# Kernel tuning notes

Hardware: AMD Instinct MI355X
Metric: run time of the kernel (lower is better)

## Reference

```python
import jax, jax.numpy as jnp
import numpy as np

H_MODEL = 1024
N_HEADS = 16
N_KV_HEADS = 4
HEAD_DIM = 64
SLIDING_WINDOW = 512
B, S = 2, 2048
NEG_INF = -1e9


def rotate_half(x):
    half = x.shape[-1] // 2
    return jnp.concatenate([-x[..., half:], x[..., :half]], axis=-1)


def setup_inputs() -> dict:
    key = jax.random.key(0)
    ks = jax.random.split(key, 8)
    hidden_states = jax.random.normal(ks[0], (B, S, H_MODEL), dtype=jnp.float32)
    # RoPE tables (HF style): cos/sin of shape [1, S, head_dim]
    inv_freq = 1.0 / (10000.0 ** (jnp.arange(0, HEAD_DIM, 2, dtype=jnp.float32) / HEAD_DIM))
    pos = jnp.arange(S, dtype=jnp.float32)
    freqs = jnp.einsum('s,d->sd', pos, inv_freq)            # [S, D/2]
    emb = jnp.concatenate([freqs, freqs], axis=-1)          # [S, D]
    cos = jnp.cos(emb)[None]                                # [1, S, D]
    sin = jnp.sin(emb)[None]
    # additive causal + sliding-window mask [1,1,S,S]
    i = jnp.arange(S)[:, None]
    j = jnp.arange(S)[None, :]
    allowed = (j <= i) & (i - j < SLIDING_WINDOW)
    attention_mask = jnp.where(allowed, 0.0, NEG_INF).astype(jnp.float32)[None, None]
    # projection weights (torch Linear stores [out, in]; y = x @ W.T)
    std = 0.02
    Wq = jax.random.normal(ks[1], (N_HEADS * HEAD_DIM, H_MODEL), dtype=jnp.float32) * std
    Wk = jax.random.normal(ks[2], (N_KV_HEADS * HEAD_DIM, H_MODEL), dtype=jnp.float32) * std
    Wv = jax.random.normal(ks[3], (N_KV_HEADS * HEAD_DIM, H_MODEL), dtype=jnp.float32) * std
    Wo = jax.random.normal(ks[4], (H_MODEL, N_HEADS * HEAD_DIM), dtype=jnp.float32) * std
    return {"hidden_states": hidden_states, "cos": cos, "sin": sin,
            "attention_mask": attention_mask, "Wq": Wq, "Wk": Wk, "Wv": Wv, "Wo": Wo}


def reference(hidden_states, cos, sin, attention_mask, Wq, Wk, Wv, Wo):
    b, s, _ = hidden_states.shape
    G = N_HEADS // N_KV_HEADS
    scaling = HEAD_DIM ** -0.5
    # QKV projections -> [B, H, S, D]
    q = jnp.einsum('bsh,oh->bso', hidden_states, Wq).reshape(b, s, N_HEADS, HEAD_DIM).transpose(0, 2, 1, 3)
    k = jnp.einsum('bsh,oh->bso', hidden_states, Wk).reshape(b, s, N_KV_HEADS, HEAD_DIM).transpose(0, 2, 1, 3)
    v = jnp.einsum('bsh,oh->bso', hidden_states, Wv).reshape(b, s, N_KV_HEADS, HEAD_DIM).transpose(0, 2, 1, 3)
    # RoPE (cos/sin broadcast over head dim via unsqueeze(1))
    c = cos[:, None, :, :]
    sn = sin[:, None, :, :]
    q = q * c + rotate_half(q) * sn
    k = k * c + rotate_half(k) * sn
    # GQA eager attention: group query heads over kv heads
    qg = q.reshape(b, N_KV_HEADS, G, s, HEAD_DIM)
    scores = jnp.einsum('bkgqd,bkpd->bkgqp', qg, k) * scaling  # [B,Hkv,G,S,S]
    scores = scores + attention_mask[:, :, None, :, :]
    probs = jax.nn.softmax(scores.astype(jnp.float32), axis=-1).astype(q.dtype)
    out = jnp.einsum('bkgqp,bkpd->bkgqd', probs, v)            # [B,Hkv,G,S,D]
    out = out.reshape(b, N_HEADS, s, HEAD_DIM).transpose(0, 2, 1, 3).reshape(b, s, N_HEADS * HEAD_DIM)
    return jnp.einsum('bso,ho->bsh', out, Wo)
```

## Files before the change

kernel.cpp:

```cpp
#include <hip/hip_runtime.h>
#include <hip/hip_bf16.h>

#define S_LEN 2048
#define NH 16
#define NKV 4
#define HD 64
#define WIN 512
#define BATCH 2

typedef __bf16 bf16_8 __attribute__((ext_vector_type(8)));
typedef __bf16 bf16_4 __attribute__((ext_vector_type(4)));
typedef float f32x4 __attribute__((ext_vector_type(4)));

__device__ inline bf16_8 cvt8(f32x4 a, f32x4 b) {
    bf16_8 r;
    r[0] = (__bf16)a[0]; r[1] = (__bf16)a[1]; r[2] = (__bf16)a[2]; r[3] = (__bf16)a[3];
    r[4] = (__bf16)b[0]; r[5] = (__bf16)b[1]; r[6] = (__bf16)b[2]; r[7] = (__bf16)b[3];
    return r;
}

__global__ __launch_bounds__(256) void cvt_pack(
    const float* __restrict__ hs, const float* __restrict__ Wq,
    const float* __restrict__ Wk, const float* __restrict__ Wv,
    const float* __restrict__ Wo,
    __bf16* __restrict__ hsb, __bf16* __restrict__ Wqp,
    __bf16* __restrict__ Wkp, __bf16* __restrict__ Wvp,
    __bf16* __restrict__ Wop)
{
    int i = blockIdx.x * 256 + threadIdx.x;
    if (i < 524288) {
        const size_t j = (size_t)i * 8;
        const f32x4 a = *(const f32x4*)(hs + j);
        const f32x4 b = *(const f32x4*)(hs + j + 4);
        *(bf16_8*)(hsb + j) = cvt8(a, b);
        return;
    }
    i -= 524288;
    const float* S; __bf16* P;
    if (i < 131072)      { S = Wq; P = Wqp; }
    else if (i < 163840) { S = Wk; P = Wkp; i -= 131072; }
    else if (i < 196608) { S = Wv; P = Wvp; i -= 163840; }
    else                 { S = Wo; P = Wop; i -= 196608; }
    const int n = i >> 7;
    const int k = (i & 127) << 3;
    const f32x4 a = *(const f32x4*)(S + (size_t)n * 1024 + k);
    const f32x4 b = *(const f32x4*)(S + (size_t)n * 1024 + k + 4);
    const size_t dst = ((size_t)((n >> 4) * 32 + (k >> 5)) << 9)
                     + ((size_t)((n & 15) | (((k >> 3) & 3) << 4)) << 3);
    *(bf16_8*)(P + dst) = cvt8(a, b);
}

#define GEMM_K_LOOP(Ap_, Bq_, row0_)                                           \
    const int ar = tid >> 2, ac = (tid & 3) << 4;                              \
    const int fm = lane & 15;                                                  \
    const int fj = (lane >> 4) << 3;                                           \
    const f32x4 fzero = {0.f, 0.f, 0.f, 0.f};                                  \
    f32x4 acc[2][4];                                                           \
    _Pragma("unroll") for (int i = 0; i < 2; ++i)                              \
        _Pragma("unroll") for (int nt = 0; nt < 4; ++nt) acc[i][nt] = fzero;   \
    const size_t aoff = (size_t)(row0_ + ar) * 1024 + ac;                      \
    bf16_8 b0[4], b1[4];                                                       \
    {                                                                          \
        const bf16_8 a0 = *(const bf16_8*)&Ap_[aoff];                          \
        const bf16_8 a1 = *(const bf16_8*)&Ap_[aoff + 8];                      \
        *(bf16_8*)&As[ar * 72 + ac]     = a0;                                  \
        *(bf16_8*)&As[ar * 72 + ac + 8] = a1;                                  \
        _Pragma("unroll") for (int nt = 0; nt < 4; ++nt)                       \
            b0[nt] = *(const bf16_8*)(Bq_ + nt * 16384);                       \
    }                                                                          \
    __syncthreads();                                                           \
    for (int it = 0; it < 16; ++it) {                                          \
        const int cur = it & 1;                                                \
        const bool pf = it < 15;                                               \
        bf16_8 qa0, qa1, bn[4];                                                \
        if (pf) {                                                              \
            qa0 = *(const bf16_8*)&Ap_[aoff + (it + 1) * 64];                  \
            qa1 = *(const bf16_8*)&Ap_[aoff + (it + 1) * 64 + 8];              \
        }                                                                      \
        _Pragma("unroll") for (int nt = 0; nt < 4; ++nt)                       \
            b1[nt] = *(const bf16_8*)(Bq_ + nt * 16384 + (it * 2 + 1) * 512);  \
        bf16_8 af0[2];                                                         \
        _Pragma("unroll") for (int i = 0; i < 2; ++i)                          \
            af0[i] = *(const bf16_8*)&As[cur * 4608 + (wm * 32 + i * 16 + fm) * 72 + fj]; \
        _Pragma("unroll") for (int i = 0; i < 2; ++i)                          \
            _Pragma("unroll") for (int nt = 0; nt < 4; ++nt)                   \
                acc[i][nt] = __builtin_amdgcn_mfma_f32_16x16x32_bf16(          \
                    af0[i], b0[nt], acc[i][nt], 0, 0, 0);                      \
        if (pf) {                                                              \
            _Pragma("unroll") for (int nt = 0; nt < 4; ++nt)                   \
                bn[nt] = *(const bf16_8*)(Bq_ + nt * 16384 + (it + 1) * 1024); \
        }                                                                      \
        bf16_8 af1[2];                                                         \
        _Pragma("unroll") for (int i = 0; i < 2; ++i)                          \
            af1[i] = *(const bf16_8*)&As[cur * 4608 + (wm * 32 + i * 16 + fm) * 72 + 32 + fj]; \
        _Pragma("unroll") for (int i = 0; i < 2; ++i)                          \
            _Pragma("unroll") for (int nt = 0; nt < 4; ++nt)                   \
                acc[i][nt] = __builtin_amdgcn_mfma_f32_16x16x32_bf16(          \
                    af1[i], b1[nt], acc[i][nt], 0, 0, 0);                      \
        if (pf) {                                                              \
            const int nb = cur ^ 1;                                            \
            *(bf16_8*)&As[nb * 4608 + ar * 72 + ac]     = qa0;                 \
            *(bf16_8*)&As[nb * 4608 + ar * 72 + ac + 8] = qa1;                 \
            _Pragma("unroll") for (int nt = 0; nt < 4; ++nt) b0[nt] = bn[nt];  \
        }                                                                      \
        __syncthreads();                                                       \
    }                                                                          \
    const int drow = (lane >> 4) << 2;

__global__ __launch_bounds__(256) void gemm_qkv(
    const __bf16* __restrict__ A,
    const __bf16* __restrict__ Wqp,
    const __bf16* __restrict__ Wkp,
    const __bf16* __restrict__ Wvp,
    __bf16* __restrict__ Qb,
    __bf16* __restrict__ Kb,
    __bf16* __restrict__ Vt,
    const float* __restrict__ cosb,
    const float* __restrict__ sinb)
{
    __shared__ __align__(16) __bf16 smem[9216];
    __bf16* const As = smem;

    const int tid  = threadIdx.x;
    const int wave = tid >> 6;
    const int lane = tid & 63;
    const int wm   = wave & 1;
    const int wn   = wave >> 1;

    const int row0 = blockIdx.x * 64;
    const int by   = blockIdx.y;

    const __bf16* Bp; int colb; int mode;
    __bf16* C; int ldc; int col0;
    if (by < 8)       { Bp = Wqp; colb = by * 128;        C = Qb; ldc = 1024; col0 = by * 128;        mode = 0; }
    else if (by < 10) { Bp = Wkp; colb = (by - 8) * 128;  C = Kb; ldc = 256;  col0 = (by - 8) * 128;  mode = 1; }
    else              { Bp = Wvp; colb = (by - 10) * 128; C = 0;  ldc = 0;    col0 = (by - 10) * 128; mode = 2; }

    const __bf16* Bq = Bp + (size_t)((colb + wn * 64) >> 4) * 16384 + (lane << 3);

    GEMM_K_LOOP(A, Bq, row0)

    const int cq = col0 + wn * 64;
    if (mode < 2) {
#pragma unroll
        for (int i = 0; i < 2; ++i) {
#pragma unroll
            for (int r = 0; r < 4; ++r) {
                const int row = row0 + wm * 32 + i * 16 + drow + r;
                const int s   = row & (S_LEN - 1);
#pragma unroll
                for (int nt = 0; nt < 2; ++nt) {
                    const int d = nt * 16 + fm;
                    const float c1 = cosb[s * HD + d];
                    const float s1 = sinb[s * HD + d];
                    const float c2 = cosb[s * HD + d + 32];
                    const float s2 = sinb[s * HD + d + 32];
                    const float x1 = acc[i][nt][r];
                    const float x2 = acc[i][nt + 2][r];
                    C[(size_t)row * ldc + cq + d]      = (__bf16)(x1 * c1 - x2 * s1);
                    C[(size_t)row * ldc + cq + d + 32] = (__bf16)(x2 * c2 + x1 * s2);
                }
            }
        }
    } else {
        __bf16* T = smem;
#pragma unroll
        for (int i = 0; i < 2; ++i)
#pragma unroll
            for (int r = 0; r < 4; ++r)
#pragma unroll
                for (int nt = 0; nt < 4; ++nt)
                    T[(wn * 64 + nt * 16 + fm) * 72 + wm * 32 + i * 16 + drow + r] =
                        (__bf16)acc[i][nt][r];
        __syncthreads();
        const int nl = tid >> 1;
        const int so = (tid & 1) << 5;
        const int ng = col0 + nl;
        const int kh = ng >> 6, d = ng & 63;
        const int b  = row0 >> 11, s0v = row0 & (S_LEN - 1);
        __bf16* dst = &Vt[(size_t)((b * NKV + kh) * HD + d) * S_LEN + s0v + so];
#pragma unroll
        for (int c = 0; c < 4; ++c)
            *(bf16_8*)(dst + c * 8) = *(const bf16_8*)&T[nl * 72 + so + c * 8];
    }
}

__global__ __launch_bounds__(256) void gemm_o(
    const __bf16* __restrict__ A,
    const __bf16* __restrict__ Bp,
    float* __restrict__ C)
{
    __shared__ __align__(16) __bf16 smem[9216];
    __bf16* const As = smem;

    const int tid  = threadIdx.x;
    const int wave = tid >> 6;
    const int lane = tid & 63;
    const int wm   = wave & 1;
    const int wn   = wave >> 1;

    const int row0 = blockIdx.x * 64;
    const int colb = blockIdx.y * 128;

    const __bf16* Bq = Bp + (size_t)((colb + wn * 64) >> 4) * 16384 + (lane << 3);

    GEMM_K_LOOP(A, Bq, row0)

#pragma unroll
    for (int i = 0; i < 2; ++i)
#pragma unroll
        for (int r = 0; r < 4; ++r) {
            const int row = row0 + wm * 32 + i * 16 + drow + r;
#pragma unroll
            for (int nt = 0; nt < 4; ++nt)
                C[(size_t)row * 1024 + colb + wn * 64 + nt * 16 + fm] = acc[i][nt][r];
        }
}

__global__ __launch_bounds__(256) void attn_mfma(const __bf16* __restrict__ Q,
                                                 const __bf16* __restrict__ K,
                                                 const __bf16* __restrict__ Vt,
                                                 __bf16* __restrict__ O)
{
    __shared__ __align__(16) __bf16 Ks[64 * 72];
    __shared__ __align__(16) __bf16 Vs[64 * 72];
    __shared__ __align__(16) __bf16 Ps[4][16][72];

    const int tid  = threadIdx.x;
    const int wave = tid >> 6;
    const int lane = tid & 63;

    const int qt = blockIdx.x & (S_LEN / 64 - 1);
    const int h  = (blockIdx.x >> 5) & (NH - 1);
    const int b  = blockIdx.x >> 9;
    const int kh = h >> 2;

    const int q0 = qt * 64;
    const int qw = q0 + wave * 16;

    const int fm = lane & 15;
    const int fj = (lane >> 4) << 3;

    const size_t qrow = (size_t)(b * S_LEN + qw + fm) * (NH * HD) + h * HD;
    const bf16_8 qf0 = *(const bf16_8*)&Q[qrow + fj];
    const bf16_8 qf1 = *(const bf16_8*)&Q[qrow + 32 + fj];

    const f32x4 fzero = {0.f, 0.f, 0.f, 0.f};
    f32x4 oacc[4];
    float l[4];
#pragma unroll
    for (int nt = 0; nt < 4; ++nt) oacc[nt] = fzero;
#pragma unroll
    for (int r = 0; r < 4; ++r) l[r] = 0.f;

    const int kr = tid >> 3;
    const int kc = (tid & 7) << 3;
    const size_t kbase = (size_t)(b * S_LEN + kr) * (NKV * HD) + kh * HD + kc;
    const size_t vbase = (size_t)((b * NKV + kh) * HD + kr) * S_LEN + kc;
    const int qbase = qw + ((lane >> 4) << 2);

    const int lo  = (q0 >= WIN) ? (q0 - WIN) : 0;
    const int nit = ((q0 - lo) >> 6) + 1;

    bf16_8 pk0 = *(const bf16_8*)&K[kbase + (size_t)lo * (NKV * HD)];
    bf16_8 pk1 = *(const bf16_8*)&K[kbase + (size_t)(lo + 32) * (NKV * HD)];
    bf16_8 pv0 = *(const bf16_8*)&Vt[vbase + lo];
    bf16_8 pv1 = *(const bf16_8*)&Vt[vbase + (size_t)32 * S_LEN + lo];

    for (int it = 0; it < nit; ++it) {
        const int kb = lo + (it << 6);
        *(bf16_8*)&Ks[kr * 72 + kc]        = pk0;
        *(bf16_8*)&Ks[(kr + 32) * 72 + kc] = pk1;
        *(bf16_8*)&Vs[kr * 72 + kc]        = pv0;
        *(bf16_8*)&Vs[(kr + 32) * 72 + kc] = pv1;
        __syncthreads();

        if (it + 1 < nit) {
            const int kn = kb + 64;
            pk0 = *(const bf16_8*)&K[kbase + (size_t)kn * (NKV * HD)];
            pk1 = *(const bf16_8*)&K[kbase + (size_t)(kn + 32) * (NKV * HD)];
            pv0 = *(const bf16_8*)&Vt[vbase + kn];
            pv1 = *(const bf16_8*)&Vt[vbase + (size_t)32 * S_LEN + kn];
        }

        if (kb <= qw + 15 && (qw - kb) < (WIN + 63)) {
            f32x4 sc[4];
#pragma unroll
            for (int t = 0; t < 4; ++t) {
                const bf16_8 klo = *(const bf16_8*)&Ks[(t * 16 + fm) * 72 + fj];
                const bf16_8 khi = *(const bf16_8*)&Ks[(t * 16 + fm) * 72 + 32 + fj];
                f32x4 s = fzero;
                s = __builtin_amdgcn_mfma_f32_16x16x32_bf16(qf0, klo, s, 0, 0, 0);
                s = __builtin_amdgcn_mfma_f32_16x16x32_bf16(qf1, khi, s, 0, 0, 0);
                sc[t] = s;
            }

#pragma unroll
            for (int t = 0; t < 4; ++t) {
                const int ki = kb + t * 16 + fm;
#pragma unroll
                for (int r = 0; r < 4; ++r) {
                    const int qr = qbase + r;
                    const float e = __expf(sc[t][r] * 0.125f);
                    const float p = (ki <= qr && qr - ki < WIN) ? e : 0.f;
                    l[r] += p;
                    Ps[wave][((lane >> 4) << 2) + r][t * 16 + fm] = (__bf16)p;
                }
            }

            const bf16_8 pf0 = *(const bf16_8*)&Ps[wave][fm][fj];
            const bf16_8 pf1 = *(const bf16_8*)&Ps[wave][fm][32 + fj];
#pragma unroll
            for (int nt = 0; nt < 4; ++nt) {
                const bf16_8 vlo = *(const bf16_8*)&Vs[(nt * 16 + fm) * 72 + fj];
                const bf16_8 vhi = *(const bf16_8*)&Vs[(nt * 16 + fm) * 72 + 32 + fj];
                oacc[nt] = __builtin_amdgcn_mfma_f32_16x16x32_bf16(pf0, vlo, oacc[nt], 0, 0, 0);
                oacc[nt] = __builtin_amdgcn_mfma_f32_16x16x32_bf16(pf1, vhi, oacc[nt], 0, 0, 0);
            }
        }
        __syncthreads();
    }

#pragma unroll
    for (int off = 8; off > 0; off >>= 1)
#pragma unroll
        for (int r = 0; r < 4; ++r)
            l[r] += __shfl_xor(l[r], off, 64);

    const int drow = (lane >> 4) << 2;
    float inv[4];
#pragma unroll
    for (int r = 0; r < 4; ++r) inv[r] = 1.0f / l[r];
#pragma unroll
    for (int nt = 0; nt < 4; ++nt)
#pragma unroll
        for (int r = 0; r < 4; ++r) {
            const size_t off = (size_t)(b * S_LEN + qw + drow + r) * (NH * HD) + h * HD + nt * 16 + fm;
            O[off] = (__bf16)(oacc[nt][r] * inv[r]);
        }
}

extern "C" void kernel_launch(void* const* d_in, const int* in_sizes, int n_in,
                              void* d_out, int out_size, void* d_ws, size_t ws_size,
                              hipStream_t stream)
{
    const float* hs   = (const float*)d_in[0];
    const float* cosb = (const float*)d_in[1];
    const float* sinb = (const float*)d_in[2];
    const float* Wq = (const float*)d_in[4];
    const float* Wk = (const float*)d_in[5];
    const float* Wv = (const float*)d_in[6];
    const float* Wo = (const float*)d_in[7];

    const int M = BATCH * S_LEN;

    __bf16* hsb = (__bf16*)d_ws;
    __bf16* Wqp = hsb + (size_t)M * 1024;
    __bf16* Wkp = Wqp + 1024 * 1024;
    __bf16* Wvp = Wkp + 256 * 1024;
    __bf16* Wop = Wvp + 256 * 1024;
    __bf16* Qb  = Wop + 1024 * 1024;
    __bf16* Kb  = Qb  + (size_t)M * 1024;
    __bf16* Vtb = Kb  + (size_t)M * 256;
    __bf16* Ob  = Vtb + (size_t)M * 256;

    dim3 blk(256);
    cvt_pack<<<3328, blk, 0, stream>>>(hs, Wq, Wk, Wv, Wo,
                                       hsb, Wqp, Wkp, Wvp, Wop);

    gemm_qkv<<<dim3(64, 12), blk, 0, stream>>>(hsb, Wqp, Wkp, Wvp,
                                               Qb, Kb, Vtb, cosb, sinb);

    attn_mfma<<<BATCH * NH * (S_LEN / 64), blk, 0, stream>>>(Qb, Kb, Vtb, Ob);

    gemm_o<<<dim3(64, 8), blk, 0, stream>>>(Ob, Wop, (float*)d_out);
}
```

Baseline: 160.6 us.

## Fuse all four kernels into one persistent cooperative kernel with grid syncs

Replaces the four launches (convert/pack, QKV GEMM with RoPE, attention, output GEMM) with a single cooperative kernel of 512 persistent blocks. The stages are separated by grid.sync() and each block loops over tiles. The aim is to remove per-launch overhead and the idle gaps between kernels. In exchange, the grid is fixed at 512 blocks, so the attention stage runs 4 tiles serially per block and load balance changes. Grid-wide barriers cost something, and occupancy is constrained by launch_bounds(256,2) and a larger shared-memory footprint.

```diff
diff --git a/kernel.cpp b/kernel.cpp
--- a/kernel.cpp
+++ b/kernel.cpp
@@ -1,5 +1,8 @@
 #include <hip/hip_runtime.h>
 #include <hip/hip_bf16.h>
+#include <hip/hip_cooperative_groups.h>
+
+namespace cg = cooperative_groups;
 
 #define S_LEN 2048
 #define NH 16
@@ -7,9 +10,9 @@
 #define HD 64
 #define WIN 512
 #define BATCH 2
+#define GRID 512
 
 typedef __bf16 bf16_8 __attribute__((ext_vector_type(8)));
-typedef __bf16 bf16_4 __attribute__((ext_vector_type(4)));
 typedef float f32x4 __attribute__((ext_vector_type(4)));
 
 __device__ inline bf16_8 cvt8(f32x4 a, f32x4 b) {
@@ -19,325 +22,325 @@
     return r;
 }
 
-__global__ __launch_bounds__(256) void cvt_pack(
-    const float* __restrict__ hs, const float* __restrict__ Wq,
-    const float* __restrict__ Wk, const float* __restrict__ Wv,
-    const float* __restrict__ Wo,
+__device__ __forceinline__ void gemm64x128(
+    const __bf16* __restrict__ Ap, const __bf16* __restrict__ Bq,
+    int row0, __bf16* __restrict__ As, int tid, f32x4 acc[2][4])
+{
+    const int wave = tid >> 6;
+    const int lane = tid & 63;
+    const int wm   = wave & 1;
+    const int ar = tid >> 2, ac = (tid & 3) << 4;
+    const int fm = lane & 15;
+    const int fj = (lane >> 4) << 3;
+    const f32x4 fzero = {0.f, 0.f, 0.f, 0.f};
+#pragma unroll
+    for (int i = 0; i < 2; ++i)
+#pragma unroll
+        for (int nt = 0; nt < 4; ++nt) acc[i][nt] = fzero;
+
+    const size_t aoff = (size_t)(row0 + ar) * 1024 + ac;
+    bf16_8 b0[4], b1[4];
+    {
+        const bf16_8 a0 = *(const bf16_8*)&Ap[aoff];
+        const bf16_8 a1 = *(const bf16_8*)&Ap[aoff + 8];
+        *(bf16_8*)&As[ar * 72 + ac]     = a0;
+        *(bf16_8*)&As[ar * 72 + ac + 8] = a1;
+#pragma unroll
+        for (int nt = 0; nt < 4; ++nt)
+            b0[nt] = *(const bf16_8*)(Bq + nt * 16384);
+    }
+    __syncthreads();
+
+    for (int it = 0; it < 16; ++it) {
+        const int cur = it & 1;
+        const bool pf = it < 15;
+        bf16_8 qa0, qa1, bn[4];
+        if (pf) {
+            qa0 = *(const bf16_8*)&Ap[aoff + (it + 1) * 64];
+            qa1 = *(const bf16_8*)&Ap[aoff + (it + 1) * 64 + 8];
+        }
+#pragma unroll
+        for (int nt = 0; nt < 4; ++nt)
+            b1[nt] = *(const bf16_8*)(Bq + nt * 16384 + (it * 2 + 1) * 512);
+
+        bf16_8 af0[2];
+#pragma unroll
+        for (int i = 0; i < 2; ++i)
+            af0[i] = *(const bf16_8*)&As[cur * 4608 + (wm * 32 + i * 16 + fm) * 72 + fj];
+#pragma unroll
+        for (int i = 0; i < 2; ++i)
+#pragma unroll
+            for (int nt = 0; nt < 4; ++nt)
+                acc[i][nt] = __builtin_amdgcn_mfma_f32_16x16x32_bf16(af0[i], b0[nt], acc[i][nt], 0, 0, 0);
+
+        if (pf) {
+#pragma unroll
+            for (int nt = 0; nt < 4; ++nt)
+                bn[nt] = *(const bf16_8*)(Bq + nt * 16384 + (it + 1) * 1024);
+        }
+        bf16_8 af1[2];
+#pragma unroll
+        for (int i = 0; i < 2; ++i)
+            af1[i] = *(const bf16_8*)&As[cur * 4608 + (wm * 32 + i * 16 + fm) * 72 + 32 + fj];
+#pragma unroll
+        for (int i = 0; i < 2; ++i)
+#pragma unroll
+            for (int nt = 0; nt < 4; ++nt)
+                acc[i][nt] = __builtin_amdgcn_mfma_f32_16x16x32_bf16(af1[i], b1[nt], acc[i][nt], 0, 0, 0);
+
+        if (pf) {
+            const int nb = cur ^ 1;
+            *(bf16_8*)&As[nb * 4608 + ar * 72 + ac]     = qa0;
+            *(bf16_8*)&As[nb * 4608 + ar * 72 + ac + 8] = qa1;
+#pragma unroll
+            for (int nt = 0; nt < 4; ++nt) b0[nt] = bn[nt];
+        }
+        __syncthreads();
+    }
+}
+
+__global__ __launch_bounds__(256, 2) void fused_all(
+    const float* __restrict__ hs,  const float* __restrict__ cosb,
+    const float* __restrict__ sinb,
+    const float* __restrict__ Wq,  const float* __restrict__ Wk,
+    const float* __restrict__ Wv,  const float* __restrict__ Wo,
     __bf16* __restrict__ hsb, __bf16* __restrict__ Wqp,
     __bf16* __restrict__ Wkp, __bf16* __restrict__ Wvp,
-    __bf16* __restrict__ Wop)
+    __bf16* __restrict__ Wop,
+    __bf16* __restrict__ Qb,  __bf16* __restrict__ Kb,
+    __bf16* __restrict__ Vt,  __bf16* __restrict__ Ob,
+    float* __restrict__ outp)
 {
-    int i = blockIdx.x * 256 + threadIdx.x;
-    if (i < 524288) {
-        const size_t j = (size_t)i * 8;
-        const f32x4 a = *(const f32x4*)(hs + j);
-        const f32x4 b = *(const f32x4*)(hs + j + 4);
-        *(bf16_8*)(hsb + j) = cvt8(a, b);
-        return;
-    }
-    i -= 524288;
-    const float* S; __bf16* P;
-    if (i < 131072)      { S = Wq; P = Wqp; }
-    else if (i < 163840) { S = Wk; P = Wkp; i -= 131072; }
-    else if (i < 196608) { S = Wv; P = Wvp; i -= 163840; }
-    else                 { S = Wo; P = Wop; i -= 196608; }
-    const int n = i >> 7;
-    const int k = (i & 127) << 3;
-    const f32x4 a = *(const f32x4*)(S + (size_t)n * 1024 + k);
-    const f32x4 b = *(const f32x4*)(S + (size_t)n * 1024 + k + 4);
-    const size_t dst = ((size_t)((n >> 4) * 32 + (k >> 5)) << 9)
-                     + ((size_t)((n & 15) | (((k >> 3) & 3) << 4)) << 3);
-    *(bf16_8*)(P + dst) = cvt8(a, b);
-}
-
-#define GEMM_K_LOOP(Ap_, Bq_, row0_)                                           \
-    const int ar = tid >> 2, ac = (tid & 3) << 4;                              \
-    const int fm = lane & 15;                                                  \
-    const int fj = (lane >> 4) << 3;                                           \
-    const f32x4 fzero = {0.f, 0.f, 0.f, 0.f};                                  \
-    f32x4 acc[2][4];                                                           \
-    _Pragma("unroll") for (int i = 0; i < 2; ++i)                              \
-        _Pragma("unroll") for (int nt = 0; nt < 4; ++nt) acc[i][nt] = fzero;   \
-    const size_t aoff = (size_t)(row0_ + ar) * 1024 + ac;                      \
-    bf16_8 b0[4], b1[4];                                                       \
-    {                                                                          \
-        const bf16_8 a0 = *(const bf16_8*)&Ap_[aoff];                          \
-        const bf16_8 a1 = *(const bf16_8*)&Ap_[aoff + 8];                      \
-        *(bf16_8*)&As[ar * 72 + ac]     = a0;                                  \
-        *(bf16_8*)&As[ar * 72 + ac + 8] = a1;                                  \
-        _Pragma("unroll") for (int nt = 0; nt < 4; ++nt)                       \
-            b0[nt] = *(const bf16_8*)(Bq_ + nt * 16384);                       \
-    }                                                                          \
-    __syncthreads();                                                           \
-    for (int it = 0; it < 16; ++it) {                                          \
-        const int cur = it & 1;                                                \
-        const bool pf = it < 15;                                               \
-        bf16_8 qa0, qa1, bn[4];                                                \
-        if (pf) {                                                              \
-            qa0 = *(const bf16_8*)&Ap_[aoff + (it + 1) * 64];                  \
-            qa1 = *(const bf16_8*)&Ap_[aoff + (it + 1) * 64 + 8];              \
-        }                                                                      \
-        _Pragma("unroll") for (int nt = 0; nt < 4; ++nt)                       \
-            b1[nt] = *(const bf16_8*)(Bq_ + nt * 16384 + (it * 2 + 1) * 512);  \
-        bf16_8 af0[2];                                                         \
-        _Pragma("unroll") for (int i = 0; i < 2; ++i)                          \
-            af0[i] = *(const bf16_8*)&As[cur * 4608 + (wm * 32 + i * 16 + fm) * 72 + fj]; \
-        _Pragma("unroll") for (int i = 0; i < 2; ++i)                          \
-            _Pragma("unroll") for (int nt = 0; nt < 4; ++nt)                   \
-                acc[i][nt] = __builtin_amdgcn_mfma_f32_16x16x32_bf16(          \
-                    af0[i], b0[nt], acc[i][nt], 0, 0, 0);                      \
-        if (pf) {                                                              \
-            _Pragma("unroll") for (int nt = 0; nt < 4; ++nt)                   \
-                bn[nt] = *(const bf16_8*)(Bq_ + nt * 16384 + (it + 1) * 1024); \
-        }                                                                      \
-        bf16_8 af1[2];                                                         \
-        _Pragma("unroll") for (int i = 0; i < 2; ++i)                          \
-            af1[i] = *(const bf16_8*)&As[cur * 4608 + (wm * 32 + i * 16 + fm) * 72 + 32 + fj]; \
-        _Pragma("unroll") for (int i = 0; i < 2; ++i)                          \
-            _Pragma("unroll") for (int nt = 0; nt < 4; ++nt)                   \
-                acc[i][nt] = __builtin_amdgcn_mfma_f32_16x16x32_bf16(          \
-                    af1[i], b1[nt], acc[i][nt], 0, 0, 0);                      \
-        if (pf) {                                                              \
-            const int nb = cur ^ 1;                                            \
-            *(bf16_8*)&As[nb * 4608 + ar * 72 + ac]     = qa0;                 \
-            *(bf16_8*)&As[nb * 4608 + ar * 72 + ac + 8] = qa1;                 \
-            _Pragma("unroll") for (int nt = 0; nt < 4; ++nt) b0[nt] = bn[nt];  \
-        }                                                                      \
-        __syncthreads();                                                       \
-    }                                                                          \
-    const int drow = (lane >> 4) << 2;
-
-__global__ __launch_bounds__(256) void gemm_qkv(
-    const __bf16* __restrict__ A,
-    const __bf16* __restrict__ Wqp,
-    const __bf16* __restrict__ Wkp,
-    const __bf16* __restrict__ Wvp,
-    __bf16* __restrict__ Qb,
-    __bf16* __restrict__ Kb,
-    __bf16* __restrict__ Vt,
-    const float* __restrict__ cosb,
-    const float* __restrict__ sinb)
-{
-    __shared__ __align__(16) __bf16 smem[9216];
-    __bf16* const As = smem;
+    __shared__ __align__(16) __bf16 smem[13824];
+    cg::grid_group grid = cg::this_grid();
 
     const int tid  = threadIdx.x;
+    const int bid  = blockIdx.x;
     const int wave = tid >> 6;
     const int lane = tid & 63;
     const int wm   = wave & 1;
     const int wn   = wave >> 1;
-
-    const int row0 = blockIdx.x * 64;
-    const int by   = blockIdx.y;
-
-    const __bf16* Bp; int colb; int mode;
-    __bf16* C; int ldc; int col0;
-    if (by < 8)       { Bp = Wqp; colb = by * 128;        C = Qb; ldc = 1024; col0 = by * 128;        mode = 0; }
-    else if (by < 10) { Bp = Wkp; colb = (by - 8) * 128;  C = Kb; ldc = 256;  col0 = (by - 8) * 128;  mode = 1; }
-    else              { Bp = Wvp; colb = (by - 10) * 128; C = 0;  ldc = 0;    col0 = (by - 10) * 128; mode = 2; }
-
-    const __bf16* Bq = Bp + (size_t)((colb + wn * 64) >> 4) * 16384 + (lane << 3);
-
-    GEMM_K_LOOP(A, Bq, row0)
-
-    const int cq = col0 + wn * 64;
-    if (mode < 2) {
-#pragma unroll
-        for (int i = 0; i < 2; ++i) {
+    const int fm   = lane & 15;
+    const int fj   = (lane >> 4) << 3;
+
+    for (int i0 = bid * 256 + tid; i0 < 851968; i0 += GRID * 256) {
+        int i = i0;
+        if (i < 524288) {
+            const size_t j = (size_t)i * 8;
+            const f32x4 a = *(const f32x4*)(hs + j);
+            const f32x4 b = *(const f32x4*)(hs + j + 4);
+            *(bf16_8*)(hsb + j) = cvt8(a, b);
+            continue;
+        }
+        i -= 524288;
+        const float* S; __bf16* P;
+        if (i < 131072)      { S = Wq; P = Wqp; }
+        else if (i < 163840) { S = Wk; P = Wkp; i -= 131072; }
+        else if (i < 196608) { S = Wv; P = Wvp; i -= 163840; }
+        else                 { S = Wo; P = Wop; i -= 196608; }
+        const int n = i >> 7;
+        const int k = (i & 127) << 3;
+        const f32x4 a = *(const f32x4*)(S + (size_t)n * 1024 + k);
+        const f32x4 b = *(const f32x4*)(S + (size_t)n * 1024 + k + 4);
+        const size_t dst = ((size_t)((n >> 4) * 32 + (k >> 5)) << 9)
+                         + ((size_t)((n & 15) | (((k >> 3) & 3) << 4)) << 3);
+        *(bf16_8*)(P + dst) = cvt8(a, b);
+    }
+    grid.sync();
+
+    for (int t = bid; t < 768; t += GRID) {
+        const int row0 = (t & 63) * 64;
+        const int by   = t >> 6;
+
+        const __bf16* Bp; int colb; int mode;
+        __bf16* C; int ldc; int col0;
+        if (by < 8)       { Bp = Wqp; colb = by * 128;        C = Qb; ldc = 1024; col0 = by * 128;        mode = 0; }
+        else if (by < 10) { Bp = Wkp; colb = (by - 8) * 128;  C = Kb; ldc = 256;  col0 = (by - 8) * 128;  mode = 1; }
+        else              { Bp = Wvp; colb = (by - 10) * 128; C = 0;  ldc = 0;    col0 = (by - 10) * 128; mode = 2; }
+
+        const __bf16* Bq = Bp + (size_t)((colb + wn * 64) >> 4) * 16384 + (lane << 3);
+        f32x4 acc[2][4];
+        gemm64x128(hsb, Bq, row0, smem, tid, acc);
+
+        const int drow = (lane >> 4) << 2;
+        const int cq   = col0 + wn * 64;
+        if (mode < 2) {
+#pragma unroll
+            for (int i = 0; i < 2; ++i) {
+#pragma unroll
+                for (int r = 0; r < 4; ++r) {
+                    const int row = row0 + wm * 32 + i * 16 + drow + r;
+                    const int s   = row & (S_LEN - 1);
+#pragma unroll
+                    for (int nt = 0; nt < 2; ++nt) {
+                        const int d = nt * 16 + fm;
+                        const float c1 = cosb[s * HD + d];
+                        const float s1 = sinb[s * HD + d];
+                        const float c2 = cosb[s * HD + d + 32];
+                        const float s2 = sinb[s * HD + d + 32];
+                        const float x1 = acc[i][nt][r];
+                        const float x2 = acc[i][nt + 2][r];
+                        C[(size_t)row * ldc + cq + d]      = (__bf16)(x1 * c1 - x2 * s1);
+                        C[(size_t)row * ldc + cq + d + 32] = (__bf16)(x2 * c2 + x1 * s2);
+                    }
+                }
+            }
+        } else {
+            __bf16* T = smem;
+#pragma unroll
+            for (int i = 0; i < 2; ++i)
+#pragma unroll
+                for (int r = 0; r < 4; ++r)
+#pragma unroll
+                    for (int nt = 0; nt < 4; ++nt)
+                        T[(wn * 64 + nt * 16 + fm) * 72 + wm * 32 + i * 16 + drow + r] =
+                            (__bf16)acc[i][nt][r];
+            __syncthreads();
+            const int nl = tid >> 1;
+            const int so = (tid & 1) << 5;
+            const int ng = col0 + nl;
+            const int kh = ng >> 6, d = ng & 63;
+            const int b  = row0 >> 11, s0v = row0 & (S_LEN - 1);
+            __bf16* dst = &Vt[(size_t)((b * NKV + kh) * HD + d) * S_LEN + s0v + so];
+#pragma unroll
+            for (int c = 0; c < 4; ++c)
+                *(bf16_8*)(dst + c * 8) = *(const bf16_8*)&T[nl * 72 + so + c * 8];
+        }
+        __syncthreads();
+    }
+    grid.sync();
+
+    {
+        __bf16* const Ks = smem;
+        __bf16* const Vs = smem + 4608;
+        __bf16* const Ps = smem + 9216;
+
+        for (int t = bid * 4; t < bid * 4 + 4; ++t) {
+            const int qt = t & (S_LEN / 64 - 1);
+            const int h  = (t >> 5) & (NH - 1);
+            const int b  = t >> 9;
+            const int kh = h >> 2;
+
+            const int q0 = qt * 64;
+            const int qw = q0 + wave * 16;
+
+            const size_t qrow = (size_t)(b * S_LEN + qw + fm) * (NH * HD) + h * HD;
+            const bf16_8 qf0 = *(const bf16_8*)&Qb[qrow + fj];
+            const bf16_8 qf1 = *(const bf16_8*)&Qb[qrow + 32 + fj];
+
+            const f32x4 fzero = {0.f, 0.f, 0.f, 0.f};
+            f32x4 oacc[4];
+            float l[4];
+#pragma unroll
+            for (int nt = 0; nt < 4; ++nt) oacc[nt] = fzero;
+#pragma unroll
+            for (int r = 0; r < 4; ++r) l[r] = 0.f;
+
+            const int kr = tid >> 3;
+            const int kc = (tid & 7) << 3;
+            const size_t kbase = (size_t)(b * S_LEN + kr) * (NKV * HD) + kh * HD + kc;
+            const size_t vbase = (size_t)((b * NKV + kh) * HD + kr) * S_LEN + kc;
+            const int qbase = qw + ((lane >> 4) << 2);
+
+            const int lo  = (q0 >= WIN) ? (q0 - WIN) : 0;
+            const int nit = ((q0 - lo) >> 6) + 1;
+
+            bf16_8 pk0 = *(const bf16_8*)&Kb[kbase + (size_t)lo * (NKV * HD)];
+            bf16_8 pk1 = *(const bf16_8*)&Kb[kbase + (size_t)(lo + 32) * (NKV * HD)];
+            bf16_8 pv0 = *(const bf16_8*)&Vt[vbase + lo];
+            bf16_8 pv1 = *(const bf16_8*)&Vt[vbase + (size_t)32 * S_LEN + lo];
+
+            for (int it = 0; it < nit; ++it) {
+                const int kb = lo + (it << 6);
+                *(bf16_8*)&Ks[kr * 72 + kc]        = pk0;
+                *(bf16_8*)&Ks[(kr + 32) * 72 + kc] = pk1;
+                *(bf16_8*)&Vs[kr * 72 + kc]        = pv0;
+                *(bf16_8*)&Vs[(kr + 32) * 72 + kc] = pv1;
+                __syncthreads();
+
+                if (it + 1 < nit) {
+                    const int kn = kb + 64;
+                    pk0 = *(const bf16_8*)&Kb[kbase + (size_t)kn * (NKV * HD)];
+                    pk1 = *(const bf16_8*)&Kb[kbase + (size_t)(kn + 32) * (NKV * HD)];
+                    pv0 = *(const bf16_8*)&Vt[vbase + kn];
+                    pv1 = *(const bf16_8*)&Vt[vbase + (size_t)32 * S_LEN + kn];
+                }
+
+                if (kb <= qw + 15 && (qw - kb) < (WIN + 63)) {
+                    f32x4 sc[4];
+#pragma unroll
+                    for (int tt = 0; tt < 4; ++tt) {
+                        const bf16_8 klo = *(const bf16_8*)&Ks[(tt * 16 + fm) * 72 + fj];
+                        const bf16_8 khi = *(const bf16_8*)&Ks[(tt * 16 + fm) * 72 + 32 + fj];
+                        f32x4 s = fzero;
+                        s = __builtin_amdgcn_mfma_f32_16x16x32_bf16(qf0, klo, s, 0, 0, 0);
+                        s = __builtin_amdgcn_mfma_f32_16x16x32_bf16(qf1, khi, s, 0, 0, 0);
+                        sc[tt] = s;
+                    }
+#pragma unroll
+                    for (int tt = 0; tt < 4; ++tt) {
+                        const int ki = kb + tt * 16 + fm;
+#pragma unroll
+                        for (int r = 0; r < 4; ++r) {
+                            const int qr = qbase + r;
+                            const float e = __expf(sc[tt][r] * 0.125f);
+                            const float p = (ki <= qr && qr - ki < WIN) ? e : 0.f;
+                            l[r] += p;
+                            Ps[(wave * 16 + ((lane >> 4) << 2) + r) * 72 + tt * 16 + fm] = (__bf16)p;
+                        }
+                    }
+                    const bf16_8 pf0 = *(const bf16_8*)&Ps[(wave * 16 + fm) * 72 + fj];
+                    const bf16_8 pf1 = *(const bf16_8*)&Ps[(wave * 16 + fm) * 72 + 32 + fj];
+#pragma unroll
+                    for (int nt = 0; nt < 4; ++nt) {
+                        const bf16_8 vlo = *(const bf16_8*)&Vs[(nt * 16 + fm) * 72 + fj];
+                        const bf16_8 vhi = *(const bf16_8*)&Vs[(nt * 16 + fm) * 72 + 32 + fj];
+                        oacc[nt] = __builtin_amdgcn_mfma_f32_16x16x32_bf16(pf0, vlo, oacc[nt], 0, 0, 0);
+                        oacc[nt] = __builtin_amdgcn_mfma_f32_16x16x32_bf16(pf1, vhi, oacc[nt], 0, 0, 0);
+                    }
+                }
+                __syncthreads();
+            }
+
+#pragma unroll
+            for (int off = 8; off > 0; off >>= 1)
+#pragma unroll
+                for (int r = 0; r < 4; ++r)
+                    l[r] += __shfl_xor(l[r], off, 64);
+
+            const int drow = (lane >> 4) << 2;
+            float inv[4];
+#pragma unroll
+            for (int r = 0; r < 4; ++r) inv[r] = 1.0f / l[r];
+#pragma unroll
+            for (int nt = 0; nt < 4; ++nt)
+#pragma unroll
+                for (int r = 0; r < 4; ++r) {
+                    const size_t off = (size_t)(b * S_LEN + qw + drow + r) * (NH * HD) + h * HD + nt * 16 + fm;
+                    Ob[off] = (__bf16)(oacc[nt][r] * inv[r]);
+                }
+        }
+    }
+    grid.sync();
+
+    {
+        const int row0 = (bid & 63) * 64;
+        const int colb = (bid >> 6) * 128;
+        const __bf16* Bq = Wop + (size_t)((colb + wn * 64) >> 4) * 16384 + (lane << 3);
+        f32x4 acc[2][4];
+        gemm64x128(Ob, Bq, row0, smem, tid, acc);
+
+        const int drow = (lane >> 4) << 2;
+#pragma unroll
+        for (int i = 0; i < 2; ++i)
 #pragma unroll
             for (int r = 0; r < 4; ++r) {
                 const int row = row0 + wm * 32 + i * 16 + drow + r;
-                const int s   = row & (S_LEN - 1);
-#pragma unroll
-                for (int nt = 0; nt < 2; ++nt) {
-                    const int d = nt * 16 + fm;
-                    const float c1 = cosb[s * HD + d];
-                    const float s1 = sinb[s * HD + d];
-                    const float c2 = cosb[s * HD + d + 32];
-                    const float s2 = sinb[s * HD + d + 32];
-                    const float x1 = acc[i][nt][r];
-                    const float x2 = acc[i][nt + 2][r];
-                    C[(size_t)row * ldc + cq + d]      = (__bf16)(x1 * c1 - x2 * s1);
-                    C[(size_t)row * ldc + cq + d + 32] = (__bf16)(x2 * c2 + x1 * s2);
-                }
+#pragma unroll
+                for (int nt = 0; nt < 4; ++nt)
+                    outp[(size_t)row * 1024 + colb + wn * 64 + nt * 16 + fm] = acc[i][nt][r];
             }
-        }
-    } else {
-        __bf16* T = smem;
-#pragma unroll
-        for (int i = 0; i < 2; ++i)
-#pragma unroll
-            for (int r = 0; r < 4; ++r)
-#pragma unroll
-                for (int nt = 0; nt < 4; ++nt)
-                    T[(wn * 64 + nt * 16 + fm) * 72 + wm * 32 + i * 16 + drow + r] =
-                        (__bf16)acc[i][nt][r];
-        __syncthreads();
-        const int nl = tid >> 1;
-        const int so = (tid & 1) << 5;
-        const int ng = col0 + nl;
-        const int kh = ng >> 6, d = ng & 63;
-        const int b  = row0 >> 11, s0v = row0 & (S_LEN - 1);
-        __bf16* dst = &Vt[(size_t)((b * NKV + kh) * HD + d) * S_LEN + s0v + so];
-#pragma unroll
-        for (int c = 0; c < 4; ++c)
-            *(bf16_8*)(dst + c * 8) = *(const bf16_8*)&T[nl * 72 + so + c * 8];
-    }
-}
-
-__global__ __launch_bounds__(256) void gemm_o(
-    const __bf16* __restrict__ A,
-    const __bf16* __restrict__ Bp,
-    float* __restrict__ C)
-{
-    __shared__ __align__(16) __bf16 smem[9216];
-    __bf16* const As = smem;
-
-    const int tid  = threadIdx.x;
-    const int wave = tid >> 6;
-    const int lane = tid & 63;
-    const int wm   = wave & 1;
-    const int wn   = wave >> 1;
-
-    const int row0 = blockIdx.x * 64;
-    const int colb = blockIdx.y * 128;
-
-    const __bf16* Bq = Bp + (size_t)((colb + wn * 64) >> 4) * 16384 + (lane << 3);
-
-    GEMM_K_LOOP(A, Bq, row0)
-
-#pragma unroll
-    for (int i = 0; i < 2; ++i)
-#pragma unroll
-        for (int r = 0; r < 4; ++r) {
-            const int row = row0 + wm * 32 + i * 16 + drow + r;
-#pragma unroll
-            for (int nt = 0; nt < 4; ++nt)
-                C[(size_t)row * 1024 + colb + wn * 64 + nt * 16 + fm] = acc[i][nt][r];
-        }
-}
-
-__global__ __launch_bounds__(256) void attn_mfma(const __bf16* __restrict__ Q,
-                                                 const __bf16* __restrict__ K,
-                                                 const __bf16* __restrict__ Vt,
-                                                 __bf16* __restrict__ O)
-{
-    __shared__ __align__(16) __bf16 Ks[64 * 72];
-    __shared__ __align__(16) __bf16 Vs[64 * 72];
-    __shared__ __align__(16) __bf16 Ps[4][16][72];
-
-    const int tid  = threadIdx.x;
-    const int wave = tid >> 6;
-    const int lane = tid & 63;
-
-    const int qt = blockIdx.x & (S_LEN / 64 - 1);
-    const int h  = (blockIdx.x >> 5) & (NH - 1);
-    const int b  = blockIdx.x >> 9;
-    const int kh = h >> 2;
-
-    const int q0 = qt * 64;
-    const int qw = q0 + wave * 16;
-
-    const int fm = lane & 15;
-    const int fj = (lane >> 4) << 3;
-
-    const size_t qrow = (size_t)(b * S_LEN + qw + fm) * (NH * HD) + h * HD;
-    const bf16_8 qf0 = *(const bf16_8*)&Q[qrow + fj];
-    const bf16_8 qf1 = *(const bf16_8*)&Q[qrow + 32 + fj];
-
-    const f32x4 fzero = {0.f, 0.f, 0.f, 0.f};
-    f32x4 oacc[4];
-    float l[4];
-#pragma unroll
-    for (int nt = 0; nt < 4; ++nt) oacc[nt] = fzero;
-#pragma unroll
-    for (int r = 0; r < 4; ++r) l[r] = 0.f;
-
-    const int kr = tid >> 3;
-    const int kc = (tid & 7) << 3;
-    const size_t kbase = (size_t)(b * S_LEN + kr) * (NKV * HD) + kh * HD + kc;
-    const size_t vbase = (size_t)((b * NKV + kh) * HD + kr) * S_LEN + kc;
-    const int qbase = qw + ((lane >> 4) << 2);
-
-    const int lo  = (q0 >= WIN) ? (q0 - WIN) : 0;
-    const int nit = ((q0 - lo) >> 6) + 1;
-
-    bf16_8 pk0 = *(const bf16_8*)&K[kbase + (size_t)lo * (NKV * HD)];
-    bf16_8 pk1 = *(const bf16_8*)&K[kbase + (size_t)(lo + 32) * (NKV * HD)];
-    bf16_8 pv0 = *(const bf16_8*)&Vt[vbase + lo];
-    bf16_8 pv1 = *(const bf16_8*)&Vt[vbase + (size_t)32 * S_LEN + lo];
-
-    for (int it = 0; it < nit; ++it) {
-        const int kb = lo + (it << 6);
-        *(bf16_8*)&Ks[kr * 72 + kc]        = pk0;
-        *(bf16_8*)&Ks[(kr + 32) * 72 + kc] = pk1;
-        *(bf16_8*)&Vs[kr * 72 + kc]        = pv0;
-        *(bf16_8*)&Vs[(kr + 32) * 72 + kc] = pv1;
-        __syncthreads();
-
-        if (it + 1 < nit) {
-            const int kn = kb + 64;
-            pk0 = *(const bf16_8*)&K[kbase + (size_t)kn * (NKV * HD)];
-            pk1 = *(const bf16_8*)&K[kbase + (size_t)(kn + 32) * (NKV * HD)];
-            pv0 = *(const bf16_8*)&Vt[vbase + kn];
-            pv1 = *(const bf16_8*)&Vt[vbase + (size_t)32 * S_LEN + kn];
-        }
-
-        if (kb <= qw + 15 && (qw - kb) < (WIN + 63)) {
-            f32x4 sc[4];
-#pragma unroll
-            for (int t = 0; t < 4; ++t) {
-                const bf16_8 klo = *(const bf16_8*)&Ks[(t * 16 + fm) * 72 + fj];
-                const bf16_8 khi = *(const bf16_8*)&Ks[(t * 16 + fm) * 72 + 32 + fj];
-                f32x4 s = fzero;
-                s = __builtin_amdgcn_mfma_f32_16x16x32_bf16(qf0, klo, s, 0, 0, 0);
-                s = __builtin_amdgcn_mfma_f32_16x16x32_bf16(qf1, khi, s, 0, 0, 0);
-                sc[t] = s;
-            }
-
-#pragma unroll
-            for (int t = 0; t < 4; ++t) {
-                const int ki = kb + t * 16 + fm;
-#pragma unroll
-                for (int r = 0; r < 4; ++r) {
-                    const int qr = qbase + r;
-                    const float e = __expf(sc[t][r] * 0.125f);
-                    const float p = (ki <= qr && qr - ki < WIN) ? e : 0.f;
-                    l[r] += p;
-                    Ps[wave][((lane >> 4) << 2) + r][t * 16 + fm] = (__bf16)p;
-                }
-            }
-
-            const bf16_8 pf0 = *(const bf16_8*)&Ps[wave][fm][fj];
-            const bf16_8 pf1 = *(const bf16_8*)&Ps[wave][fm][32 + fj];
-#pragma unroll
-            for (int nt = 0; nt < 4; ++nt) {
-                const bf16_8 vlo = *(const bf16_8*)&Vs[(nt * 16 + fm) * 72 + fj];
-                const bf16_8 vhi = *(const bf16_8*)&Vs[(nt * 16 + fm) * 72 + 32 + fj];
-                oacc[nt] = __builtin_amdgcn_mfma_f32_16x16x32_bf16(pf0, vlo, oacc[nt], 0, 0, 0);
-                oacc[nt] = __builtin_amdgcn_mfma_f32_16x16x32_bf16(pf1, vhi, oacc[nt], 0, 0, 0);
-            }
-        }
-        __syncthreads();
-    }
-
-#pragma unroll
-    for (int off = 8; off > 0; off >>= 1)
-#pragma unroll
-        for (int r = 0; r < 4; ++r)
-            l[r] += __shfl_xor(l[r], off, 64);
-
-    const int drow = (lane >> 4) << 2;
-    float inv[4];
-#pragma unroll
-    for (int r = 0; r < 4; ++r) inv[r] = 1.0f / l[r];
-#pragma unroll
-    for (int nt = 0; nt < 4; ++nt)
-#pragma unroll
-        for (int r = 0; r < 4; ++r) {
-            const size_t off = (size_t)(b * S_LEN + qw + drow + r) * (NH * HD) + h * HD + nt * 16 + fm;
-            O[off] = (__bf16)(oacc[nt][r] * inv[r]);
-        }
+    }
 }
 
 extern "C" void kernel_launch(void* const* d_in, const int* in_sizes, int n_in,
@@ -363,15 +366,14 @@
     __bf16* Kb  = Qb  + (size_t)M * 1024;
     __bf16* Vtb = Kb  + (size_t)M * 256;
     __bf16* Ob  = Vtb + (size_t)M * 256;
-
-    dim3 blk(256);
-    cvt_pack<<<3328, blk, 0, stream>>>(hs, Wq, Wk, Wv, Wo,
-                                       hsb, Wqp, Wkp, Wvp, Wop);
-
-    gemm_qkv<<<dim3(64, 12), blk, 0, stream>>>(hsb, Wqp, Wkp, Wvp,
-                                               Qb, Kb, Vtb, cosb, sinb);
-
-    attn_mfma<<<BATCH * NH * (S_LEN / 64), blk, 0, stream>>>(Qb, Kb, Vtb, Ob);
-
-    gemm_o<<<dim3(64, 8), blk, 0, stream>>>(Ob, Wop, (float*)d_out);
+    float*  outp = (float*)d_out;
+
+    void* args[] = {
+        (void*)&hs, (void*)&cosb, (void*)&sinb,
+        (void*)&Wq, (void*)&Wk, (void*)&Wv, (void*)&Wo,
+        (void*)&hsb, (void*)&Wqp, (void*)&Wkp, (void*)&Wvp, (void*)&Wop,
+        (void*)&Qb, (void*)&Kb, (void*)&Vtb, (void*)&Ob, (void*)&outp
+    };
+    hipLaunchCooperativeKernel((const void*)fused_all, dim3(GRID), dim3(256),
+                               args, 0, stream);
 }
```

Result: slower. 402.7 us (+150.8%).
